# Optimization experiments

Hardware: AMD Instinct MI355X
Metric: run time of the kernel (lower is better)

The kernel has to match this reference:

```python
import jax, jax.numpy as jnp
import numpy as np

B, S, D = 4, 4096, 256


def _complex_linear(x_r, x_i, w_r, w_i):
    # torch nn.Linear: y = x @ W.T ; complex mult: (Wr + i Wi)(xr + i xi)
    real = x_r @ w_r.T - x_i @ w_i.T
    imag = x_i @ w_r.T + x_r @ w_i.T
    return real, imag


def setup_inputs() -> dict:
    key = jax.random.key(0)
    ks = jax.random.split(key, 8)
    std = 1.0 / np.sqrt(D)  # ~ nn.Linear default init scale
    return {
        "query_real": jax.random.normal(ks[0], (B, S, D), jnp.float32),
        "query_imag": jax.random.normal(ks[1], (B, S, D), jnp.float32),
        "wq_real": jax.random.normal(ks[2], (D, D), jnp.float32) * std,
        "wq_imag": jax.random.normal(ks[3], (D, D), jnp.float32) * std,
        "wk_real": jax.random.normal(ks[4], (D, D), jnp.float32) * std,
        "wk_imag": jax.random.normal(ks[5], (D, D), jnp.float32) * std,
        "wv_real": jax.random.normal(ks[6], (D, D), jnp.float32) * std,
        "wv_imag": jax.random.normal(ks[7], (D, D), jnp.float32) * std,
    }


def reference(query_real, query_imag, wq_real, wq_imag, wk_real, wk_imag, wv_real, wv_imag):
    dim = query_real.shape[-1]
    scale = dim ** (-0.5)  # faithful: uses dim, not 2*dim

    q_r, q_i = _complex_linear(query_real, query_imag, wq_real, wq_imag)
    k_r, k_i = _complex_linear(query_real, query_imag, wk_real, wk_imag)
    v_r, v_i = _complex_linear(query_real, query_imag, wv_real, wv_imag)

    q_flat = jnp.concatenate([q_r, q_i], axis=-1)  # [B,S,2D]
    k_flat = jnp.concatenate([k_r, k_i], axis=-1)  # [B,S,2D]

    scores = jnp.einsum('bqd,bkd->bqk', q_flat, k_flat) * scale  # [B,S,S]
    attn = jax.nn.softmax(scores, axis=-1)

    out_r = jnp.einsum('bqk,bkd->bqd', attn, v_r)
    out_i = jnp.einsum('bqk,bkd->bqd', attn, v_i)
    return out_r, out_i, attn
```

## Files before the change

### kernel.cpp

```cpp
#include <hip/hip_runtime.h>
#include <hip/hip_fp16.h>

typedef _Float16 f16;
typedef _Float16 f16x8 __attribute__((ext_vector_type(8)));
typedef _Float16 f16x4 __attribute__((ext_vector_type(4)));
typedef float f32x4 __attribute__((ext_vector_type(4)));

#define AS1 __attribute__((address_space(1)))
#define AS3 __attribute__((address_space(3)))

__device__ __forceinline__ void g2l16(const void* g, void* l) {
  __builtin_amdgcn_global_load_lds((const AS1 void*)g, (AS3 void*)l, 16, 0, 0);
}

__device__ __forceinline__ void xcd_swz(int& bx, int& by, int& bz) {
  int gx = gridDim.x, gy = gridDim.y;
  int nwg = gx * gy * gridDim.z;
  int lin = (blockIdx.z * gy + blockIdx.y) * gx + blockIdx.x;
  int swz = (lin & 7) * (nwg >> 3) + (lin >> 3);
  bx = swz % gx;
  int t = swz / gx;
  by = t % gy;
  bz = t / gy;
}

__global__ __launch_bounds__(256) void build_x(const float* __restrict__ qr,
                                               const float* __restrict__ qi,
                                               f16* __restrict__ X) {
  long i = (long)blockIdx.x * 256 + threadIdx.x;
  long e = i * 4;
  int m = (int)(e >> 9);
  int k = (int)(e & 511);
  const float* src = (k < 256) ? (qr + (long)m * 256 + k)
                               : (qi + (long)m * 256 + (k - 256));
  float4 v = *(const float4*)src;
  f16x4 h = {(f16)v.x, (f16)v.y, (f16)v.z, (f16)v.w};
  *(f16x4*)(X + e) = h;
}

__global__ __launch_bounds__(256) void build_w(const float* __restrict__ wqr,
                                               const float* __restrict__ wqi,
                                               const float* __restrict__ wkr,
                                               const float* __restrict__ wki,
                                               const float* __restrict__ wvr,
                                               const float* __restrict__ wvi,
                                               f16* __restrict__ W) {
  long i = (long)blockIdx.x * 256 + threadIdx.x;
  long e = i * 4;
  int n = (int)(e >> 9);
  int k = (int)(e & 511);
  int sel = n >> 8;
  int row = n & 255;
  int k2 = k & 255;
  bool hi = (k >= 256);
  const float *Wr, *Wi;
  if ((sel >> 1) == 0)      { Wr = wqr; Wi = wqi; }
  else if ((sel >> 1) == 1) { Wr = wkr; Wi = wki; }
  else                      { Wr = wvr; Wi = wvi; }
  const float* src;
  float sgn = 1.0f;
  if ((sel & 1) == 0) {
    if (!hi) src = Wr + (long)row * 256 + k2;
    else   { src = Wi + (long)row * 256 + k2; sgn = -1.0f; }
  } else {
    if (!hi) src = Wi + (long)row * 256 + k2;
    else     src = Wr + (long)row * 256 + k2;
  }
  float4 v = *(const float4*)src;
  f16x4 h = {(f16)(sgn * v.x), (f16)(sgn * v.y), (f16)(sgn * v.z), (f16)(sgn * v.w)};
  *(f16x4*)(W + e) = h;
}

template <int MODE>
__global__ __launch_bounds__(256) void gemm_nt(const f16* __restrict__ A, int lda, long astr,
                                               const f16* __restrict__ B, int ldb, long bstr,
                                               int K, float scale,
                                               void* __restrict__ C0, long cstr) {
  __shared__ __align__(16) f16 As[128 * 64];
  __shared__ __align__(16) f16 Bs[128 * 64];
  int bx, by, bz;
  xcd_swz(bx, by, bz);
  const f16* Ab = A + (long)bz * astr;
  const f16* Bb = B + (long)bz * bstr;
  const int tid = threadIdx.x;
  const int wave = tid >> 6, lane = tid & 63;
  const int bm = by * 128, bn = bx * 128;
  const int wm = (wave >> 1) * 64, wn = (wave & 1) * 64;
  const int lr = lane & 15, lg = lane >> 4;

  const int srow = wave * 8 + (lane >> 3);
  const int sk = ((lane & 7) ^ (lane >> 3)) * 8;

  f32x4 acc[4][4] = {};

  for (int kt = 0; kt < K; kt += 64) {
#pragma unroll
    for (int it = 0; it < 4; ++it) {
      int r = srow + it * 32;
      g2l16(Ab + (long)(bm + r) * lda + kt + sk, (char*)As + it * 4096 + wave * 1024);
      g2l16(Bb + (long)(bn + r) * ldb + kt + sk, (char*)Bs + it * 4096 + wave * 1024);
    }
    __syncthreads();
#pragma unroll
    for (int kk = 0; kk < 2; ++kk) {
      f16x8 af[4], bf[4];
#pragma unroll
      for (int f = 0; f < 4; ++f) {
        int slot = kk * 4 + lg;
        int sw = (slot ^ (lr & 7)) * 8;
        af[f] = *(const f16x8*)(As + (wm + f * 16 + lr) * 64 + sw);
        bf[f] = *(const f16x8*)(Bs + (wn + f * 16 + lr) * 64 + sw);
      }
#pragma unroll
      for (int fm = 0; fm < 4; ++fm)
#pragma unroll
        for (int fn = 0; fn < 4; ++fn)
          acc[fm][fn] = __builtin_amdgcn_mfma_f32_16x16x32_f16(af[fm], bf[fn], acc[fm][fn], 0, 0, 0);
    }
    __syncthreads();
  }

#pragma unroll
  for (int fm = 0; fm < 4; ++fm) {
#pragma unroll
    for (int fn = 0; fn < 4; ++fn) {
#pragma unroll
      for (int r = 0; r < 4; ++r) {
        int row = bm + wm + fm * 16 + lg * 4 + r;
        int col = bn + wn + fn * 16 + lr;
        float v = acc[fm][fn][r];
        if (MODE == 0) {
          ((f16*)C0)[(long)row * 1536 + col] = (f16)v;
        } else {
          ((float*)C0)[(long)bz * cstr + (long)row * 4096 + col] = v * scale;
        }
      }
    }
  }
}

__global__ __launch_bounds__(256) void build_vt(const f16* __restrict__ P,
                                                f16* __restrict__ VT) {
  __shared__ f16 t[64][66];
  const int tid = threadIdx.x;
  const long b = blockIdx.z;
  const f16* src = P + (b * 4096 + (long)blockIdx.x * 64) * 1536 + 1024 + blockIdx.y * 64;
#pragma unroll
  for (int it = 0; it < 16; ++it) {
    int lin = it * 256 + tid;
    int i = lin >> 6, j = lin & 63;
    t[i][j] = src[(long)i * 1536 + j];
  }
  __syncthreads();
  f16* dst = VT + (b * 512 + (long)blockIdx.y * 64) * 4096 + blockIdx.x * 64;
#pragma unroll
  for (int it = 0; it < 16; ++it) {
    int lin = it * 256 + tid;
    int i = lin >> 6, j = lin & 63;
    dst[(long)i * 4096 + j] = t[j][i];
  }
}

__global__ __launch_bounds__(256) void softmax_rows(float* __restrict__ attn) {
  float* p = attn + (long)blockIdx.x * 4096;
  const int tid = threadIdx.x;
  float4 v[4];
  float m = -1e30f;
#pragma unroll
  for (int j = 0; j < 4; ++j) {
    v[j] = *(const float4*)&p[(j * 256 + tid) * 4];
    m = fmaxf(m, fmaxf(fmaxf(v[j].x, v[j].y), fmaxf(v[j].z, v[j].w)));
  }
#pragma unroll
  for (int off = 32; off >= 1; off >>= 1) m = fmaxf(m, __shfl_xor(m, off));
  __shared__ float sm[8];
  if ((tid & 63) == 0) sm[tid >> 6] = m;
  __syncthreads();
  m = fmaxf(fmaxf(sm[0], sm[1]), fmaxf(sm[2], sm[3]));
  float s = 0.0f;
#pragma unroll
  for (int j = 0; j < 4; ++j) {
    v[j].x = __expf(v[j].x - m);
    v[j].y = __expf(v[j].y - m);
    v[j].z = __expf(v[j].z - m);
    v[j].w = __expf(v[j].w - m);
    s += v[j].x + v[j].y + v[j].z + v[j].w;
  }
#pragma unroll
  for (int off = 32; off >= 1; off >>= 1) s += __shfl_xor(s, off);
  if ((tid & 63) == 0) sm[4 + (tid >> 6)] = s;
  __syncthreads();
  s = sm[4] + sm[5] + sm[6] + sm[7];
  float inv = 1.0f / s;
#pragma unroll
  for (int j = 0; j < 4; ++j) {
    v[j].x *= inv; v[j].y *= inv; v[j].z *= inv; v[j].w *= inv;
    *(float4*)&p[(j * 256 + tid) * 4] = v[j];
  }
}

__global__ __launch_bounds__(256) void gemm_pv(const float* __restrict__ A,
                                               const f16* __restrict__ Bv,
                                               float* __restrict__ outR,
                                               float* __restrict__ outI) {
  __shared__ __align__(16) f16 As[128 * 64];
  __shared__ __align__(16) f16 Bs[128 * 64];
  int bx, by, bz;
  xcd_swz(bx, by, bz);
  const float* Ab = A + (long)bz * 4096 * 4096;
  const f16* Bb = Bv + (long)bz * 512 * 4096;
  const int tid = threadIdx.x;
  const int wave = tid >> 6, lane = tid & 63;
  const int bm = by * 128, bn = bx * 128;
  const int wm = (wave >> 1) * 64, wn = (wave & 1) * 64;
  const int lr = lane & 15, lg = lane >> 4;

  const int brow = wave * 8 + (lane >> 3);
  const int bk = ((lane & 7) ^ (lane >> 3)) * 8;
  const int arow0 = tid >> 4;
  const int ak = (tid & 15) * 4;
  const int acol16 = (tid & 15) >> 1;
  const int ahalf = (tid & 1) * 4;

  f32x4 acc[4][4] = {};

  for (int kt = 0; kt < 4096; kt += 64) {
#pragma unroll
    for (int it = 0; it < 4; ++it) {
      int r = brow + it * 32;
      g2l16(Bb + (long)(bn + r) * 4096 + kt + bk, (char*)Bs + it * 4096 + wave * 1024);
    }
#pragma unroll
    for (int it = 0; it < 8; ++it) {
      int r = arow0 + it * 16;
      float4 v = *(const float4*)&Ab[(long)(bm + r) * 4096 + kt + ak];
      f16x4 h = {(f16)v.x, (f16)v.y, (f16)v.z, (f16)v.w};
      *(f16x4*)(As + r * 64 + (acol16 ^ (r & 7)) * 8 + ahalf) = h;
    }
    __syncthreads();
#pragma unroll
    for (int kk = 0; kk < 2; ++kk) {
      f16x8 af[4], bf[4];
#pragma unroll
      for (int f = 0; f < 4; ++f) {
        int slot = kk * 4 + lg;
        int sw = (slot ^ (lr & 7)) * 8;
        af[f] = *(const f16x8*)(As + (wm + f * 16 + lr) * 64 + sw);
        bf[f] = *(const f16x8*)(Bs + (wn + f * 16 + lr) * 64 + sw);
      }
#pragma unroll
      for (int fm = 0; fm < 4; ++fm)
#pragma unroll
        for (int fn = 0; fn < 4; ++fn)
          acc[fm][fn] = __builtin_amdgcn_mfma_f32_16x16x32_f16(af[fm], bf[fn], acc[fm][fn], 0, 0, 0);
    }
    __syncthreads();
  }

#pragma unroll
  for (int fm = 0; fm < 4; ++fm) {
#pragma unroll
    for (int fn = 0; fn < 4; ++fn) {
#pragma unroll
      for (int r = 0; r < 4; ++r) {
        int row = bm + wm + fm * 16 + lg * 4 + r;
        int col = bn + wn + fn * 16 + lr;
        float v = acc[fm][fn][r];
        long o = ((long)bz * 4096 + row) * 256 + (col & 255);
        if (col < 256) outR[o] = v; else outI[o] = v;
      }
    }
  }
}

extern "C" void kernel_launch(void* const* d_in, const int* in_sizes, int n_in,
                              void* d_out, int out_size, void* d_ws, size_t ws_size,
                              hipStream_t stream) {
  const float* qr  = (const float*)d_in[0];
  const float* qi  = (const float*)d_in[1];
  const float* wqr = (const float*)d_in[2];
  const float* wqi = (const float*)d_in[3];
  const float* wkr = (const float*)d_in[4];
  const float* wki = (const float*)d_in[5];
  const float* wvr = (const float*)d_in[6];
  const float* wvi = (const float*)d_in[7];

  float* outR = (float*)d_out;
  float* outI = outR + (size_t)4 * 4096 * 256;
  float* attn = outI + (size_t)4 * 4096 * 256;

  char* ws = (char*)d_ws;
  f16* X  = (f16*)ws;
  f16* W  = (f16*)(ws + (size_t)16384 * 512 * 2);
  f16* P  = (f16*)(ws + (size_t)16384 * 512 * 2 + (size_t)1536 * 512 * 2);
  f16* VT = (f16*)(ws + (size_t)16384 * 512 * 2 + (size_t)1536 * 512 * 2 +
                   (size_t)16384 * 1536 * 2);

  build_x<<<8192, 256, 0, stream>>>(qr, qi, X);
  build_w<<<768, 256, 0, stream>>>(wqr, wqi, wkr, wki, wvr, wvi, W);

  gemm_nt<0><<<dim3(12, 128, 1), 256, 0, stream>>>(X, 512, 0L, W, 512, 0L, 512, 1.0f,
                                                   (void*)P, 0L);

  build_vt<<<dim3(64, 8, 4), 256, 0, stream>>>(P, VT);

  gemm_nt<1><<<dim3(32, 32, 4), 256, 0, stream>>>(P, 1536, (long)4096 * 1536,
                                                  P + 512, 1536, (long)4096 * 1536,
                                                  512, 0.0625f,
                                                  (void*)attn, (long)4096 * 4096);

  softmax_rows<<<16384, 256, 0, stream>>>(attn);

  gemm_pv<<<dim3(4, 32, 4), 256, 0, stream>>>(attn, VT, outR, outI);
}
```

Baseline: 395.9 us.

## Fuse softmax normalization into PV GEMM using per-tile row stats from QK GEMM

The QK^T GEMM epilogue now emits per-row partial max and sum-exp for each 64-column tile. A small kernel merges these into the final row max and sum. The PV GEMM then reads raw scores, normalizes them in place, writes the final attn output, and feeds fp16 probabilities to MFMA, all in one pass. This drops the separate softmax pass and its extra read and write of the 256MB score matrix. In exchange the new PV kernel covers full N=512 per block with only 256 blocks, which lowers parallelism, and it reuses the X and W workspace for the stats buffers.

```diff
diff --git a/kernel.cpp b/kernel.cpp
--- a/kernel.cpp
+++ b/kernel.cpp
@@ -75,7 +75,8 @@
 __global__ __launch_bounds__(256) void gemm_nt(const f16* __restrict__ A, int lda, long astr,
                                                const f16* __restrict__ B, int ldb, long bstr,
                                                int K, float scale,
-                                               void* __restrict__ C0, long cstr) {
+                                               void* __restrict__ C0, long cstr,
+                                               float2* __restrict__ stats) {
   __shared__ __align__(16) f16 As[128 * 64];
   __shared__ __align__(16) f16 Bs[128 * 64];
   int bx, by, bz;
@@ -106,8 +107,7 @@
       f16x8 af[4], bf[4];
 #pragma unroll
       for (int f = 0; f < 4; ++f) {
-        int slot = kk * 4 + lg;
-        int sw = (slot ^ (lr & 7)) * 8;
+        int sw = ((kk * 4 + lg) ^ (lr & 7)) * 8;
         af[f] = *(const f16x8*)(As + (wm + f * 16 + lr) * 64 + sw);
         bf[f] = *(const f16x8*)(Bs + (wn + f * 16 + lr) * 64 + sw);
       }
@@ -137,6 +137,28 @@
       }
     }
   }
+
+  if (MODE == 1) {
+    const int nt = bx * 2 + (wn >> 6);
+#pragma unroll
+    for (int fm = 0; fm < 4; ++fm) {
+#pragma unroll
+      for (int r = 0; r < 4; ++r) {
+        float v0 = acc[fm][0][r] * scale, v1 = acc[fm][1][r] * scale;
+        float v2 = acc[fm][2][r] * scale, v3 = acc[fm][3][r] * scale;
+        float mt = fmaxf(fmaxf(v0, v1), fmaxf(v2, v3));
+#pragma unroll
+        for (int off = 8; off >= 1; off >>= 1) mt = fmaxf(mt, __shfl_xor(mt, off));
+        float lt = __expf(v0 - mt) + __expf(v1 - mt) + __expf(v2 - mt) + __expf(v3 - mt);
+#pragma unroll
+        for (int off = 8; off >= 1; off >>= 1) lt += __shfl_xor(lt, off);
+        if (lr == 0) {
+          int row = bm + wm + fm * 16 + lg * 4 + r;
+          stats[((long)bz * 4096 + row) * 64 + nt] = make_float2(mt, lt);
+        }
+      }
+    }
+  }
 }
 
 __global__ __launch_bounds__(256) void build_vt(const f16* __restrict__ P,
@@ -161,112 +183,101 @@
   }
 }
 
-__global__ __launch_bounds__(256) void softmax_rows(float* __restrict__ attn) {
-  float* p = attn + (long)blockIdx.x * 4096;
-  const int tid = threadIdx.x;
-  float4 v[4];
+__global__ __launch_bounds__(256) void merge_stats(const float2* __restrict__ stats,
+                                                   float2* __restrict__ ml) {
+  long row = (long)blockIdx.x * 256 + threadIdx.x;
+  const float2* s = stats + row * 64;
   float m = -1e30f;
-#pragma unroll
-  for (int j = 0; j < 4; ++j) {
-    v[j] = *(const float4*)&p[(j * 256 + tid) * 4];
-    m = fmaxf(m, fmaxf(fmaxf(v[j].x, v[j].y), fmaxf(v[j].z, v[j].w)));
-  }
-#pragma unroll
-  for (int off = 32; off >= 1; off >>= 1) m = fmaxf(m, __shfl_xor(m, off));
-  __shared__ float sm[8];
-  if ((tid & 63) == 0) sm[tid >> 6] = m;
-  __syncthreads();
-  m = fmaxf(fmaxf(sm[0], sm[1]), fmaxf(sm[2], sm[3]));
-  float s = 0.0f;
-#pragma unroll
-  for (int j = 0; j < 4; ++j) {
-    v[j].x = __expf(v[j].x - m);
-    v[j].y = __expf(v[j].y - m);
-    v[j].z = __expf(v[j].z - m);
-    v[j].w = __expf(v[j].w - m);
-    s += v[j].x + v[j].y + v[j].z + v[j].w;
-  }
-#pragma unroll
-  for (int off = 32; off >= 1; off >>= 1) s += __shfl_xor(s, off);
-  if ((tid & 63) == 0) sm[4 + (tid >> 6)] = s;
-  __syncthreads();
-  s = sm[4] + sm[5] + sm[6] + sm[7];
-  float inv = 1.0f / s;
-#pragma unroll
-  for (int j = 0; j < 4; ++j) {
-    v[j].x *= inv; v[j].y *= inv; v[j].z *= inv; v[j].w *= inv;
-    *(float4*)&p[(j * 256 + tid) * 4] = v[j];
-  }
-}
-
-__global__ __launch_bounds__(256) void gemm_pv(const float* __restrict__ A,
-                                               const f16* __restrict__ Bv,
-                                               float* __restrict__ outR,
-                                               float* __restrict__ outI) {
-  __shared__ __align__(16) f16 As[128 * 64];
-  __shared__ __align__(16) f16 Bs[128 * 64];
-  int bx, by, bz;
-  xcd_swz(bx, by, bz);
-  const float* Ab = A + (long)bz * 4096 * 4096;
-  const f16* Bb = Bv + (long)bz * 512 * 4096;
+#pragma unroll 8
+  for (int i = 0; i < 64; ++i) m = fmaxf(m, s[i].x);
+  float l = 0.0f;
+#pragma unroll 8
+  for (int i = 0; i < 64; ++i) l += s[i].y * __expf(s[i].x - m);
+  ml[row] = make_float2(m, l);
+}
+
+__global__ __launch_bounds__(512) void pv_fused(const float2* __restrict__ ml,
+                                                float* __restrict__ attn,
+                                                const f16* __restrict__ VT,
+                                                float* __restrict__ outR,
+                                                float* __restrict__ outI) {
+  __shared__ __align__(16) f16 Ps[64 * 64];
+  __shared__ __align__(16) f16 Bs[512 * 64];
+  int lin = blockIdx.y * 64 + blockIdx.x;
+  int swz = (lin & 7) * 32 + (lin >> 3);
+  int bx = swz & 63, b = swz >> 6;
+  const int bm = bx * 64;
+  float* Ab = attn + (long)b * 4096 * 4096;
+  const f16* Bb = VT + (long)b * 512 * 4096;
   const int tid = threadIdx.x;
   const int wave = tid >> 6, lane = tid & 63;
-  const int bm = by * 128, bn = bx * 128;
-  const int wm = (wave >> 1) * 64, wn = (wave & 1) * 64;
+  const int wm2 = (wave >> 2) * 32;
+  const int wn2 = (wave & 3) * 128;
   const int lr = lane & 15, lg = lane >> 4;
 
-  const int brow = wave * 8 + (lane >> 3);
-  const int bk = ((lane & 7) ^ (lane >> 3)) * 8;
-  const int arow0 = tid >> 4;
-  const int ak = (tid & 15) * 4;
-  const int acol16 = (tid & 15) >> 1;
-  const int ahalf = (tid & 1) * 4;
-
-  f32x4 acc[4][4] = {};
+  const int prow = tid >> 3;
+  const int pc8 = tid & 7;
+  const int vsw = ((lane & 7) ^ ((lane >> 3) & 7)) * 8;
+  float2 mlv = ml[(long)b * 4096 + bm + prow];
+  const float mrow = mlv.x;
+  const float invl = 1.0f / mlv.y;
+
+  f32x4 acc[2][8] = {};
 
   for (int kt = 0; kt < 4096; kt += 64) {
 #pragma unroll
-    for (int it = 0; it < 4; ++it) {
-      int r = brow + it * 32;
-      g2l16(Bb + (long)(bn + r) * 4096 + kt + bk, (char*)Bs + it * 4096 + wave * 1024);
-    }
-#pragma unroll
-    for (int it = 0; it < 8; ++it) {
-      int r = arow0 + it * 16;
-      float4 v = *(const float4*)&Ab[(long)(bm + r) * 4096 + kt + ak];
-      f16x4 h = {(f16)v.x, (f16)v.y, (f16)v.z, (f16)v.w};
-      *(f16x4*)(As + r * 64 + (acol16 ^ (r & 7)) * 8 + ahalf) = h;
-    }
+    for (int i = 0; i < 8; ++i) {
+      int r = i * 64 + wave * 8 + (lane >> 3);
+      g2l16(Bb + (long)r * 4096 + kt + vsw, (char*)Bs + i * 8192 + wave * 1024);
+    }
+    float* srow = Ab + (long)(bm + prow) * 4096 + kt + pc8 * 8;
+    float4 s0 = *(const float4*)srow;
+    float4 s1 = *(const float4*)(srow + 4);
+    float p0 = __expf(s0.x - mrow) * invl, p1 = __expf(s0.y - mrow) * invl;
+    float p2 = __expf(s0.z - mrow) * invl, p3 = __expf(s0.w - mrow) * invl;
+    float p4 = __expf(s1.x - mrow) * invl, p5 = __expf(s1.y - mrow) * invl;
+    float p6 = __expf(s1.z - mrow) * invl, p7 = __expf(s1.w - mrow) * invl;
+    float4 w0 = {p0, p1, p2, p3}, w1 = {p4, p5, p6, p7};
+    *(float4*)srow = w0;
+    *(float4*)(srow + 4) = w1;
+    f16x8 h = {(f16)p0, (f16)p1, (f16)p2, (f16)p3, (f16)p4, (f16)p5, (f16)p6, (f16)p7};
+    *(f16x8*)(Ps + prow * 64 + (pc8 ^ (prow & 7)) * 8) = h;
     __syncthreads();
 #pragma unroll
     for (int kk = 0; kk < 2; ++kk) {
-      f16x8 af[4], bf[4];
-#pragma unroll
-      for (int f = 0; f < 4; ++f) {
-        int slot = kk * 4 + lg;
-        int sw = (slot ^ (lr & 7)) * 8;
-        af[f] = *(const f16x8*)(As + (wm + f * 16 + lr) * 64 + sw);
-        bf[f] = *(const f16x8*)(Bs + (wn + f * 16 + lr) * 64 + sw);
-      }
-#pragma unroll
-      for (int fm = 0; fm < 4; ++fm)
-#pragma unroll
-        for (int fn = 0; fn < 4; ++fn)
-          acc[fm][fn] = __builtin_amdgcn_mfma_f32_16x16x32_f16(af[fm], bf[fn], acc[fm][fn], 0, 0, 0);
+      f16x8 af[2];
+#pragma unroll
+      for (int fm = 0; fm < 2; ++fm)
+        af[fm] = *(const f16x8*)(Ps + (wm2 + fm * 16 + lr) * 64 + ((kk * 4 + lg) ^ (lr & 7)) * 8);
+#pragma unroll
+      for (int fg = 0; fg < 2; ++fg) {
+        f16x8 bf[4];
+#pragma unroll
+        for (int f = 0; f < 4; ++f) {
+          int n = wn2 + fg * 64 + f * 16 + lr;
+          bf[f] = *(const f16x8*)(Bs + n * 64 + ((kk * 4 + lg) ^ (lr & 7)) * 8);
+        }
+#pragma unroll
+        for (int fm = 0; fm < 2; ++fm)
+#pragma unroll
+          for (int f = 0; f < 4; ++f)
+            acc[fm][fg * 4 + f] =
+                __builtin_amdgcn_mfma_f32_16x16x32_f16(af[fm], bf[f], acc[fm][fg * 4 + f], 0, 0, 0);
+      }
     }
     __syncthreads();
   }
 
 #pragma unroll
-  for (int fm = 0; fm < 4; ++fm) {
-#pragma unroll
-    for (int fn = 0; fn < 4; ++fn) {
+  for (int fm = 0; fm < 2; ++fm) {
+#pragma unroll
+    for (int fn = 0; fn < 8; ++fn) {
 #pragma unroll
       for (int r = 0; r < 4; ++r) {
-        int row = bm + wm + fm * 16 + lg * 4 + r;
-        int col = bn + wn + fn * 16 + lr;
+        int row = bm + wm2 + fm * 16 + lg * 4 + r;
+        int col = wn2 + fn * 16 + lr;
         float v = acc[fm][fn][r];
-        long o = ((long)bz * 4096 + row) * 256 + (col & 255);
+        long o = ((long)b * 4096 + row) * 256 + (col & 255);
         if (col < 256) outR[o] = v; else outI[o] = v;
       }
     }
@@ -295,21 +306,23 @@
   f16* P  = (f16*)(ws + (size_t)16384 * 512 * 2 + (size_t)1536 * 512 * 2);
   f16* VT = (f16*)(ws + (size_t)16384 * 512 * 2 + (size_t)1536 * 512 * 2 +
                    (size_t)16384 * 1536 * 2);
+  float2* stats = (float2*)X;
+  float2* ml    = (float2*)W;
 
   build_x<<<8192, 256, 0, stream>>>(qr, qi, X);
   build_w<<<768, 256, 0, stream>>>(wqr, wqi, wkr, wki, wvr, wvi, W);
 
   gemm_nt<0><<<dim3(12, 128, 1), 256, 0, stream>>>(X, 512, 0L, W, 512, 0L, 512, 1.0f,
-                                                   (void*)P, 0L);
+                                                   (void*)P, 0L, nullptr);
 
   build_vt<<<dim3(64, 8, 4), 256, 0, stream>>>(P, VT);
 
   gemm_nt<1><<<dim3(32, 32, 4), 256, 0, stream>>>(P, 1536, (long)4096 * 1536,
                                                   P + 512, 1536, (long)4096 * 1536,
                                                   512, 0.0625f,
-                                                  (void*)attn, (long)4096 * 4096);
-
-  softmax_rows<<<16384, 256, 0, stream>>>(attn);
-
-  gemm_pv<<<dim3(4, 32, 4), 256, 0, stream>>>(attn, VT, outR, outI);
-}
+                                                  (void*)attn, (long)4096 * 4096, stats);
+
+  merge_stats<<<64, 256, 0, stream>>>(stats, ml);
+
+  pv_fused<<<dim3(64, 4, 1), 512, 0, stream>>>(ml, attn, VT, outR, outI);
+}
```

Measured after the change: 478.5 us. +20.9%, slower.
